# Performance work log

Hardware: AMD Instinct MI355X
Metric: run time of the kernel (lower is better)

Reference implementation:

```python
import jax, jax.numpy as jnp
import numpy as np

PAD_ID = 0


def setup_inputs() -> dict:
    key = jax.random.key(0)
    ks = jax.random.split(key, 14)
    B, S, T = 64, 128, 32
    E = H = 512
    V = 32000
    s = 0.02
    return {
        "trg_tokens": jax.random.randint(ks[0], (B, T), 0, V),
        "src_tokens": jax.random.randint(ks[1], (B, S), 0, V),
        "encoder_out": jax.random.normal(ks[2], (S, B, 2 * H), jnp.float32),
        "hidden": jax.random.normal(ks[3], (B, H), jnp.float32),
        "embed_w": jax.random.normal(ks[4], (V, E), jnp.float32) * s,
        "attn_W": jax.random.normal(ks[5], (H, 2 * H + H), jnp.float32) * s,
        "attn_b": jnp.zeros((H,), jnp.float32),
        "v": jax.random.uniform(ks[6], (H,), jnp.float32),
        "W_ih": jax.random.normal(ks[7], (3 * H, 2 * H + E), jnp.float32) * s,
        "W_hh": jax.random.normal(ks[8], (3 * H, H), jnp.float32) * s,
        "b_ih": jnp.zeros((3 * H,), jnp.float32),
        "b_hh": jnp.zeros((3 * H,), jnp.float32),
        "out_W": jax.random.normal(ks[9], (V, 2 * H + H + E), jnp.float32) * s,
        "out_b": jnp.zeros((V,), jnp.float32),
    }


def reference(trg_tokens, src_tokens, encoder_out, hidden, embed_w, attn_W,
              attn_b, v, W_ih, W_hh, b_ih, b_hh, out_W, out_b):
    # trg_tokens: [B, T], src_tokens: [B, S] (transposed inside, as in torch)
    B, T = trg_tokens.shape
    S = src_tokens.shape[1]
    H = hidden.shape[1]
    V = out_W.shape[0]

    # Embedding with padding_idx -> zero row at PAD_ID
    emb = embed_w.at[PAD_ID].set(0.0)
    mask = (src_tokens != PAD_ID)              # [B, S]
    enc_bt = jnp.transpose(encoder_out, (1, 0, 2))  # [B, S, 2H]
    trg = trg_tokens.T                          # [T, B]

    def step(h, tok):
        x = emb[tok]                            # [B, E]
        # Bahdanau attention
        hrep = jnp.broadcast_to(h[:, None, :], (B, S, H))
        feat = jnp.concatenate([hrep, enc_bt], axis=2)      # [B, S, H+2H]
        energy = jnp.tanh(feat @ attn_W.T + attn_b)          # [B, S, H]
        scores = jnp.einsum('bsd,d->bs', energy, v)          # [B, S]
        scores = jnp.where(mask, scores, -jnp.inf)
        attn = jax.nn.softmax(scores, axis=1)                # [B, S]
        weighted = jnp.einsum('bs,bsd->bd', attn, enc_bt)    # [B, 2H]
        # GRU cell (torch gate order: r, z, n)
        rnn_in = jnp.concatenate([x, weighted], axis=1)      # [B, E+2H]
        gi = rnn_in @ W_ih.T + b_ih                          # [B, 3H]
        gh = h @ W_hh.T + b_hh                               # [B, 3H]
        i_r, i_z, i_n = jnp.split(gi, 3, axis=1)
        h_r, h_z, h_n = jnp.split(gh, 3, axis=1)
        r = jax.nn.sigmoid(i_r + h_r)
        z = jax.nn.sigmoid(i_z + h_z)
        n = jnp.tanh(i_n + r * h_n)
        h_new = (1.0 - z) * n + z * h                        # [B, H]
        # Output projection over cat(output, weighted, x)
        out_feat = jnp.concatenate([h_new, weighted, x], axis=1)  # [B, 2H+H+E]
        logits = out_feat @ out_W.T + out_b                  # [B, V]
        return h_new, logits

    # Teacher forcing ratio = 1.0: inputs are trg[0:T-1]; outputs[0] stays zero
    _, logits_seq = jax.lax.scan(step, hidden, trg[:T - 1])  # [T-1, B, V]
    outputs = jnp.concatenate(
        [jnp.zeros((1, B, V), logits_seq.dtype), logits_seq], axis=0)
    return outputs
```

## Files before the change

### kernel.cpp

```cpp
#include <hip/hip_runtime.h>

typedef __attribute__((ext_vector_type(4))) float f32x4;
typedef __attribute__((ext_vector_type(2))) float f32x2;
typedef __attribute__((ext_vector_type(8))) short s16x8;
typedef __attribute__((ext_vector_type(4))) short s16x4;

#define B_ 64
#define S_ 128
#define T_ 32
#define H_ 512
#define V_ 32000
#define NTILES 2000

#define SY_TILE 32
#define SY_SLOT 64
#define SY_DONE 192

__device__ __forceinline__ unsigned short f2bf(float f) {
  union { float f; unsigned u; } x; x.f = f;
  unsigned r = x.u + 0x7FFFu + ((x.u >> 16) & 1u);
  return (unsigned short)(r >> 16);
}
__device__ __forceinline__ float bf2f(unsigned short u) {
  union { unsigned u; float f; } x; x.u = ((unsigned)u) << 16; return x.f;
}
__device__ __forceinline__ float fast_tanh(float x) {
  float e = __expf(2.0f * x);
  return 1.0f - 2.0f / (e + 1.0f);
}
__device__ __forceinline__ float fast_sig(float x) {
  return 1.0f / (1.0f + __expf(-x));
}
__device__ __forceinline__ void gload16(const void* g, void* l) {
  __builtin_amdgcn_global_load_lds(
      (const __attribute__((address_space(1))) void*)g,
      (__attribute__((address_space(3))) void*)l, 16, 0, 0);
}
__device__ __forceinline__ void gload16nt(const void* g, void* l) {
  __builtin_amdgcn_global_load_lds(
      (const __attribute__((address_space(1))) void*)g,
      (__attribute__((address_space(3))) void*)l, 16, 0, 2);
}

__device__ __forceinline__ unsigned ald(const unsigned* p) {
  return __hip_atomic_load(p, __ATOMIC_RELAXED, __HIP_MEMORY_SCOPE_AGENT);
}
__device__ __forceinline__ void ast(unsigned* p, unsigned v) {
  __hip_atomic_store(p, v, __ATOMIC_RELAXED, __HIP_MEMORY_SCOPE_AGENT);
}
__device__ __forceinline__ void astf(float* p, float v) {
  union { unsigned u; float f; } x; x.f = v; ast((unsigned*)p, x.u);
}

__device__ __forceinline__ void phase_sync(unsigned* sync, int bid,
                                           unsigned st_ph, int nmask,
                                           unsigned wt_ph) {
  __syncthreads();
  if (threadIdx.x == 0)
    __hip_atomic_store(&sync[SY_SLOT + bid], st_ph, __ATOMIC_RELAXED,
                       __HIP_MEMORY_SCOPE_AGENT);
  if (threadIdx.x < 64) {
    const unsigned* p = &sync[SY_SLOT + (threadIdx.x & nmask)];
    while (ald(p) < wt_ph) __builtin_amdgcn_s_sleep(1);
  }
  __syncthreads();
}

template <int OUTBF>
__global__ __launch_bounds__(256) void big_gemm_k(
    const unsigned short* __restrict__ A, int lda,
    const unsigned short* __restrict__ W, const float* __restrict__ bias,
    void* __restrict__ Cv, int Mv, int N, int K) {
  __shared__ unsigned short As[128 * 32];
  __shared__ unsigned short Bs[128 * 32];
  const int t = threadIdx.x;
  const int wave = t >> 6, lane = t & 63;
  const int m0 = blockIdx.x * 128, n0 = blockIdx.y * 128;
  const int wm = (wave & 1) * 64, wn = (wave >> 1) * 64;
  const int fr = lane & 15, fq = lane >> 4;

  f32x4 acc[4][4];
#pragma unroll
  for (int i = 0; i < 4; ++i)
#pragma unroll
    for (int j = 0; j < 4; ++j) acc[i][j] = (f32x4){0.f, 0.f, 0.f, 0.f};

  const int g = (((lane & 3) ^ ((lane >> 3) & 3))) * 8;
  const size_t a_g0 = (size_t)(m0 + wave * 32 + (lane >> 2)) * lda + g;
  const size_t b_g0 = (size_t)(n0 + wave * 32 + (lane >> 2)) * K + g;
  unsigned short* As_w = As + wave * 1024;
  unsigned short* Bs_w = Bs + wave * 1024;
  const int sl = (fq ^ ((fr >> 1) & 3)) * 8;

  for (int kk = 0; kk < K; kk += 32) {
    gload16(A + a_g0 + kk, As_w);
    gload16(A + a_g0 + (size_t)16 * lda + kk, As_w + 512);
    gload16(W + b_g0 + kk, Bs_w);
    gload16(W + b_g0 + (size_t)16 * K + kk, Bs_w + 512);
    __syncthreads();
    s16x8 af[4], bfr[4];
#pragma unroll
    for (int f = 0; f < 4; ++f) {
      af[f] = *(const s16x8*)(As + (wm + f * 16 + fr) * 32 + sl);
      bfr[f] = *(const s16x8*)(Bs + (wn + f * 16 + fr) * 32 + sl);
    }
#pragma unroll
    for (int fm = 0; fm < 4; ++fm)
#pragma unroll
      for (int fn = 0; fn < 4; ++fn)
        acc[fm][fn] = __builtin_amdgcn_mfma_f32_16x16x32_bf16(af[fm], bfr[fn],
                                                              acc[fm][fn], 0, 0, 0);
    __syncthreads();
  }

#pragma unroll
  for (int fn = 0; fn < 4; ++fn) {
    int col = n0 + wn + fn * 16 + fr;
    float bv = bias[col];
#pragma unroll
    for (int fm = 0; fm < 4; ++fm) {
      int rb = m0 + wm + fm * 16 + fq * 4;
#pragma unroll
      for (int i = 0; i < 4; ++i) {
        int r = rb + i;
        if (r < Mv) {
          if (OUTBF)
            ((unsigned short*)Cv)[(size_t)r * N + col] = f2bf(acc[fm][fn][i] + bv);
          else
            ((float*)Cv)[(size_t)r * N + col] = acc[fm][fn][i] + bv;
        }
      }
    }
  }
}

__global__ __launch_bounds__(512) void fused_k(
    float* __restrict__ h, unsigned short* __restrict__ hbf_step,
    float* __restrict__ hgh_step, const unsigned short* __restrict__ Wcomb,
    const unsigned short* __restrict__ encp_bf,
    const unsigned short* __restrict__ enc_bf, const float* __restrict__ v,
    const int* __restrict__ src_tok, const unsigned short* __restrict__ Ww,
    const unsigned short* __restrict__ gix, const float* __restrict__ b_hh,
    unsigned short* __restrict__ Abf, const unsigned short* __restrict__ outW,
    const float* __restrict__ out_b, float* __restrict__ out,
    unsigned* __restrict__ sync) {
  __shared__ __align__(16) char smem[65536];
  const int t = threadIdx.x;
  const int lane = t & 63, w = t >> 6;
  const int fr = lane & 15, fq = lane >> 4;

  if (blockIdx.x < 64) {
    unsigned short* A0 = (unsigned short*)smem;
    unsigned short* A1 = (unsigned short*)(smem + 9216);
    unsigned short* W0 = (unsigned short*)(smem + 18432);
    unsigned short* W1 = (unsigned short*)(smem + 25344);
    unsigned short* Wp1 = (unsigned short*)(smem + 32256);
    float* gsm = (float*)smem;
    float* sc = (float*)(smem + 12288);
    const int j = blockIdx.x;
    const int ar = t >> 3, ak = (t & 7) * 8;
    const int p1_n0 = j * 32;
    const int rowt_p1 = w & 3, colt_p1 = w >> 2;
    const int rowt = (w < 4) ? w : (w - 4);

#pragma unroll
    for (int c = 0; c < 4; ++c) {
      int id = t * 4 + c;
      int r = id >> 6, cc = id & 63;
      s16x8 wv = *(const s16x8*)(Wcomb + (size_t)(p1_n0 + r) * 512 + cc * 8);
      *(s16x8*)(Wp1 + r * 520 + cc * 8) = wv;
    }

    const int wgate = ar >> 4, wdr = ar & 15;
    const int d0 = j * 16;
    const unsigned short* wwrow =
        Ww + (size_t)(wgate * 512 + d0 + wdr) * 1024 + ak;
    s16x8 pwreg[16];
    if (j < 32 && t < 384) {
#pragma unroll
      for (int p = 0; p < 16; ++p) pwreg[p] = *(const s16x8*)(wwrow + p * 64);
    }
    __syncthreads();

    for (int step = 0; step < 31; ++step) {
      const unsigned short* hbfS = hbf_step + (size_t)step * 64 * 512;
      unsigned short* hbfS1 = hbf_step + (size_t)(step + 1) * 64 * 512;
      float* hghS = hgh_step + (size_t)step * 64 * 2048;
      const unsigned ph = 3u * step;

      {
        s16x8 pa[8];
#pragma unroll
        for (int p = 0; p < 8; ++p)
          pa[p] = *(const s16x8*)(hbfS + ar * 512 + p * 64 + ak);
        *(s16x8*)(A0 + ar * 72 + ak) = pa[0];
        __syncthreads();
        f32x4 acc = {0.f, 0.f, 0.f, 0.f};
#pragma unroll
        for (int it = 0; it < 8; ++it) {
          unsigned short* bufR = (it & 1) ? A1 : A0;
          unsigned short* bufW = (it & 1) ? A0 : A1;
          s16x8 a0 = *(const s16x8*)(bufR + (rowt_p1 * 16 + fr) * 72 + fq * 8);
          s16x8 a1 =
              *(const s16x8*)(bufR + (rowt_p1 * 16 + fr) * 72 + 32 + fq * 8);
          if (it < 7) *(s16x8*)(bufW + ar * 72 + ak) = pa[it + 1];
          s16x8 b0 =
              *(const s16x8*)(Wp1 + (colt_p1 * 16 + fr) * 520 + it * 64 + fq * 8);
          s16x8 b1 = *(const s16x8*)(Wp1 + (colt_p1 * 16 + fr) * 520 + it * 64 +
                                     32 + fq * 8);
          acc = __builtin_amdgcn_mfma_f32_16x16x32_bf16(a0, b0, acc, 0, 0, 0);
          acc = __builtin_amdgcn_mfma_f32_16x16x32_bf16(a1, b1, acc, 0, 0, 0);
          __syncthreads();
        }
        int col = p1_n0 + colt_p1 * 16 + fr;
#pragma unroll
        for (int i = 0; i < 4; ++i)
          astf(&hghS[(rowt_p1 * 16 + fq * 4 + i) * 2048 + col], acc[i]);
      }
      phase_sync(sync, j, ph + 1, 15, ph + 1);

      {
        const int b = j;
        const float* hp = hghS + (size_t)b * 2048;
        float vh[8], hh[8];
        {
          f32x4 v0 = *(const f32x4*)(v + lane * 8);
          f32x4 v1 = *(const f32x4*)(v + lane * 8 + 4);
          f32x4 h0 = *(const f32x4*)(hp + lane * 8);
          f32x4 h1 = *(const f32x4*)(hp + lane * 8 + 4);
#pragma unroll
          for (int q = 0; q < 4; ++q) {
            vh[q] = v0[q]; vh[4 + q] = v1[q];
            hh[q] = h0[q]; hh[4 + q] = h1[q];
          }
        }
        for (int s = w * 16; s < w * 16 + 16; ++s) {
          s16x8 e =
              *(const s16x8*)(encp_bf + (size_t)(b * 128 + s) * 512 + lane * 8);
          float p = 0.f;
#pragma unroll
          for (int q = 0; q < 8; ++q)
            p += vh[q] * fast_tanh(hh[q] + bf2f((unsigned short)e[q]));
          for (int m = 32; m; m >>= 1) p += __shfl_xor(p, m);
          if (lane == 0)
            sc[s] = (src_tok[b * 128 + s] != 0) ? p : -__builtin_inff();
        }
        __syncthreads();
        if (t < 64) {
          float a0 = sc[t], a1 = sc[t + 64];
          float mx = fmaxf(a0, a1);
          for (int m = 32; m; m >>= 1) mx = fmaxf(mx, __shfl_xor(mx, m));
          float e0 = __expf(a0 - mx), e1 = __expf(a1 - mx);
          float ssum = e0 + e1;
          for (int m = 32; m; m >>= 1) ssum += __shfl_xor(ssum, m);
          float inv = 1.0f / ssum;
          sc[t] = e0 * inv;
          sc[t + 64] = e1 * inv;
        }
        __syncthreads();
        const int d = t * 2;
        float w0 = 0.f, w1 = 0.f;
#pragma unroll 16
        for (int s = 0; s < 128; ++s) {
          float a = sc[s];
          unsigned u = *(const unsigned*)(enc_bf + (size_t)(b * 128 + s) * 1024 + d);
          union { unsigned u; float f; } lo, hi;
          lo.u = u << 16; hi.u = u & 0xffff0000u;
          w0 += a * lo.f; w1 += a * hi.f;
        }
        unsigned pk = ((unsigned)f2bf(w1) << 16) | (unsigned)f2bf(w0);
        ast((unsigned*)(Abf + (size_t)(step * 64 + b) * 2048 + 512 + d), pk);
      }
      phase_sync(sync, j, ph + 2, 63, ph + 2);

      if (j < 32) {
        const int r0 = step * 64;
        const unsigned short* abrow = Abf + (size_t)(r0 + ar) * 2048 + 512 + ak;
        s16x8 pa[16];
#pragma unroll
        for (int p = 0; p < 16; ++p) pa[p] = *(const s16x8*)(abrow + p * 64);
        *(s16x8*)(A0 + ar * 72 + ak) = pa[0];
        if (t < 384) *(s16x8*)(W0 + ar * 72 + ak) = pwreg[0];
        __syncthreads();
        f32x4 acc0 = {0.f, 0.f, 0.f, 0.f}, acc1 = {0.f, 0.f, 0.f, 0.f};
#pragma unroll
        for (int it = 0; it < 16; ++it) {
          unsigned short* aR = (it & 1) ? A1 : A0;
          unsigned short* wR = (it & 1) ? W1 : W0;
          unsigned short* aW = (it & 1) ? A0 : A1;
          unsigned short* wW = (it & 1) ? W0 : W1;
          s16x8 a0 = *(const s16x8*)(aR + (rowt * 16 + fr) * 72 + fq * 8);
          s16x8 a1 = *(const s16x8*)(aR + (rowt * 16 + fr) * 72 + 32 + fq * 8);
          if (it < 15) {
            *(s16x8*)(aW + ar * 72 + ak) = pa[it + 1];
            if (t < 384) *(s16x8*)(wW + ar * 72 + ak) = pwreg[it + 1];
          }
          if (w < 4) {
            s16x8 b0 = *(const s16x8*)(wR + fr * 72 + fq * 8);
            s16x8 b1 = *(const s16x8*)(wR + fr * 72 + 32 + fq * 8);
            s16x8 c0 = *(const s16x8*)(wR + (32 + fr) * 72 + fq * 8);
            s16x8 c1 = *(const s16x8*)(wR + (32 + fr) * 72 + 32 + fq * 8);
            acc0 = __builtin_amdgcn_mfma_f32_16x16x32_bf16(a0, b0, acc0, 0, 0, 0);
            acc0 = __builtin_amdgcn_mfma_f32_16x16x32_bf16(a1, b1, acc0, 0, 0, 0);
            acc1 = __builtin_amdgcn_mfma_f32_16x16x32_bf16(a0, c0, acc1, 0, 0, 0);
            acc1 = __builtin_amdgcn_mfma_f32_16x16x32_bf16(a1, c1, acc1, 0, 0, 0);
          } else {
            s16x8 b0 = *(const s16x8*)(wR + (16 + fr) * 72 + fq * 8);
            s16x8 b1 = *(const s16x8*)(wR + (16 + fr) * 72 + 32 + fq * 8);
            acc0 = __builtin_amdgcn_mfma_f32_16x16x32_bf16(a0, b0, acc0, 0, 0, 0);
            acc0 = __builtin_amdgcn_mfma_f32_16x16x32_bf16(a1, b1, acc0, 0, 0, 0);
          }
          __syncthreads();
        }
        {
          const int colt0 = (w < 4) ? 0 : 1;
#pragma unroll
          for (int i = 0; i < 4; ++i) {
            int row = rowt * 16 + fq * 4 + i;
            gsm[row * 48 + colt0 * 16 + fr] =
                acc0[i] +
                bf2f(gix[(size_t)(r0 + row) * 1536 + colt0 * 512 + d0 + fr]);
          }
          if (w < 4) {
#pragma unroll
            for (int i = 0; i < 4; ++i) {
              int row = rowt * 16 + fq * 4 + i;
              gsm[row * 48 + 32 + fr] =
                  acc1[i] + bf2f(gix[(size_t)(r0 + row) * 1536 + 1024 + d0 + fr]);
            }
          }
        }
        __syncthreads();
        {
          int e = t * 2;
          int b = e >> 4, dd = e & 15, d = d0 + dd;
          float hv2[2];
          unsigned short hb2[2];
#pragma unroll
          for (int k = 0; k < 2; ++k) {
            float ir = gsm[b * 48 + dd + k];
            float iz = gsm[b * 48 + 16 + dd + k];
            float inn = gsm[b * 48 + 32 + dd + k];
            float hr = hghS[b * 2048 + 512 + d + k] + b_hh[d + k];
            float hz = hghS[b * 2048 + 1024 + d + k] + b_hh[512 + d + k];
            float hn = hghS[b * 2048 + 1536 + d + k] + b_hh[1024 + d + k];
            float r = fast_sig(ir + hr);
            float z = fast_sig(iz + hz);
            float n = fast_tanh(inn + r * hn);
            hv2[k] = (1.0f - z) * n + z * h[b * 512 + d + k];
            hb2[k] = f2bf(hv2[k]);
          }
          h[b * 512 + d] = hv2[0];
          h[b * 512 + d + 1] = hv2[1];
          unsigned pk = ((unsigned)hb2[1] << 16) | (unsigned)hb2[0];
          ast((unsigned*)(hbfS1 + b * 512 + d), pk);
          ast((unsigned*)(Abf + (size_t)(r0 + b) * 2048 + d), pk);
        }
      }
      phase_sync(sync, j, ph + 3, 31, ph + 3);
      if (j == 0 && t == 0) ast(&sync[SY_DONE], (unsigned)(step + 1));
    }
  }

  unsigned short* As2 = (unsigned short*)smem;
  unsigned short* Bs2 = (unsigned short*)(smem + 16384);
  unsigned* shp = (unsigned*)(smem + 65532);
  const int wr = (w >> 2) * 64, wc = (w & 3) * 64;

  int rowA[2], cgA[2], rowB[4], cgB[4];
#pragma unroll
  for (int c = 0; c < 2; ++c) {
    int id = (w * 2 + c) * 64 + lane;
    rowA[c] = id >> 3;
    cgA[c] = ((id & 7) - rowA[c]) & 7;
  }
#pragma unroll
  for (int c = 0; c < 4; ++c) {
    int id = (w * 4 + c) * 64 + lane;
    rowB[c] = id >> 3;
    cgB[c] = ((id & 7) - rowB[c]) & 7;
  }

  for (;;) {
    __syncthreads();
    if (t == 0)
      *shp = __hip_atomic_fetch_add(&sync[SY_TILE], 1u, __ATOMIC_RELAXED,
                                    __HIP_MEMORY_SCOPE_AGENT);
    __syncthreads();
    unsigned idx = *shp;
    if (idx >= NTILES) break;
    int mb = idx / 125;
    int nt = idx - mb * 125;
    int gate = mb * 2 + 1;
    if (gate > 30) gate = 30;
    unsigned need = (unsigned)gate + 1u;
    if (t == 0) {
      while (ald(&sync[SY_DONE]) < need) __builtin_amdgcn_s_sleep(32);
    }
    __syncthreads();

    const int m0 = mb * 128, n0 = nt * 256;
    f32x4 acc[4][4];
#pragma unroll
    for (int i = 0; i < 4; ++i)
#pragma unroll
      for (int jj = 0; jj < 4; ++jj) acc[i][jj] = (f32x4){0.f, 0.f, 0.f, 0.f};

    for (int kk = 0; kk < 2048; kk += 64) {
#pragma unroll
      for (int c = 0; c < 2; ++c)
        gload16(Abf + (size_t)(m0 + rowA[c]) * 2048 + kk + cgA[c] * 8,
                As2 + (w * 2 + c) * 512);
#pragma unroll
      for (int c = 0; c < 4; ++c)
        gload16nt(outW + (size_t)(n0 + rowB[c]) * 2048 + kk + cgB[c] * 8,
                  Bs2 + (w * 4 + c) * 512);
      __syncthreads();
#pragma unroll
      for (int kh = 0; kh < 2; ++kh) {
        int cg = kh * 4 + fq;
        s16x8 af[4], bf_[4];
#pragma unroll
        for (int i = 0; i < 4; ++i) {
          int rr = wr + i * 16 + fr;
          af[i] = *(const s16x8*)(As2 + rr * 64 + (((cg + rr) & 7) * 8));
        }
#pragma unroll
        for (int jj = 0; jj < 4; ++jj) {
          int rr = wc + jj * 16 + fr;
          bf_[jj] = *(const s16x8*)(Bs2 + rr * 64 + (((cg + rr) & 7) * 8));
        }
#pragma unroll
        for (int i = 0; i < 4; ++i)
#pragma unroll
          for (int jj = 0; jj < 4; ++jj)
            acc[i][jj] = __builtin_amdgcn_mfma_f32_16x16x32_bf16(
                af[i], bf_[jj], acc[i][jj], 0, 0, 0);
      }
      __syncthreads();
    }

#pragma unroll
    for (int jj = 0; jj < 4; ++jj) {
      int col = n0 + wc + jj * 16 + fr;
      float bv = out_b[col];
#pragma unroll
      for (int i = 0; i < 4; ++i) {
        int rb = m0 + wr + i * 16 + fq * 4;
#pragma unroll
        for (int ii = 0; ii < 4; ++ii) {
          int r = rb + ii;
          if (r < 1984) out[(size_t)(r + 64) * V_ + col] = acc[i][jj][ii] + bv;
        }
      }
    }
  }
}

__global__ __launch_bounds__(256) void cast_bf16_k(const float* __restrict__ src,
                                                   unsigned short* __restrict__ dst,
                                                   int n4) {
  int i = blockIdx.x * 256 + threadIdx.x;
  if (i >= n4) return;
  f32x4 f = *(const f32x4*)(src + (size_t)i * 4);
  s16x4 o;
#pragma unroll
  for (int q = 0; q < 4; ++q) o[q] = (short)f2bf(f[q]);
  *(s16x4*)(dst + (size_t)i * 4) = o;
}

__global__ __launch_bounds__(256) void enc_cast_k(const float* __restrict__ enc,
                                                  unsigned short* __restrict__ dst) {
  int i = blockIdx.x * 256 + threadIdx.x;
  int n = i * 4;
  int row = n >> 10, d = n & 1023;
  int s = row & (S_ - 1), b = row >> 7;
  f32x4 f = *(const f32x4*)(enc + ((size_t)s * B_ + b) * 1024 + d);
  s16x4 o;
#pragma unroll
  for (int q = 0; q < 4; ++q) o[q] = (short)f2bf(f[q]);
  *(s16x4*)(dst + (size_t)row * 1024 + d) = o;
}

__global__ __launch_bounds__(256) void build_wcomb_k(const float* __restrict__ aW,
                                                     const float* __restrict__ whh,
                                                     unsigned short* __restrict__ dst) {
  int idx = (blockIdx.x * 256 + threadIdx.x) * 4;
  int n = idx >> 9, k = idx & 511;
  const float* src = (n < 512) ? (aW + (size_t)n * 1536 + k)
                               : (whh + (size_t)(n - 512) * 512 + k);
  f32x4 f = *(const f32x4*)src;
  s16x4 o;
#pragma unroll
  for (int q = 0; q < 4; ++q) o[q] = (short)f2bf(f[q]);
  *(s16x4*)(dst + idx) = o;
}

__global__ __launch_bounds__(256) void build_wenc_k(const float* __restrict__ aW,
                                                    unsigned short* __restrict__ dst) {
  int idx = (blockIdx.x * 256 + threadIdx.x) * 4;
  int n = idx >> 10, k = idx & 1023;
  f32x4 f = *(const f32x4*)(aW + (size_t)n * 1536 + 512 + k);
  s16x4 o;
#pragma unroll
  for (int q = 0; q < 4; ++q) o[q] = (short)f2bf(f[q]);
  *(s16x4*)(dst + idx) = o;
}

__global__ __launch_bounds__(256) void build_wxw_k(const float* __restrict__ wih,
                                                   unsigned short* __restrict__ wx,
                                                   unsigned short* __restrict__ ww) {
  int flat = blockIdx.x * 256 + threadIdx.x;
  int n = flat / 384, c4 = (flat % 384) * 4;
  f32x4 f = *(const f32x4*)(wih + (size_t)n * 1536 + c4);
  s16x4 o;
#pragma unroll
  for (int q = 0; q < 4; ++q) o[q] = (short)f2bf(f[q]);
  if (c4 < 512)
    *(s16x4*)(wx + (size_t)n * 512 + c4) = o;
  else
    *(s16x4*)(ww + (size_t)n * 1024 + (c4 - 512)) = o;
}

__global__ __launch_bounds__(256) void hcast_k(const float* __restrict__ hidden,
                                               unsigned short* __restrict__ hbf0) {
  int i = blockIdx.x * 256 + threadIdx.x;
  f32x2 f = *(const f32x2*)(hidden + (size_t)i * 2);
  unsigned pk = ((unsigned)f2bf(f[1]) << 16) | (unsigned)f2bf(f[0]);
  *(unsigned*)(hbf0 + (size_t)i * 2) = pk;
}

__global__ __launch_bounds__(256) void xgather_k(const int* __restrict__ trg,
                                                 const float* __restrict__ embed,
                                                 unsigned short* __restrict__ Abf) {
  int row = blockIdx.x;
  int tt = row >> 6, b = row & 63;
  int tok = trg[b * T_ + tt];
  int d = threadIdx.x * 2;
  unsigned pk = 0;
  if (tok != 0) {
    f32x2 f = *(const f32x2*)(embed + (size_t)tok * H_ + d);
    pk = ((unsigned)f2bf(f[1]) << 16) | (unsigned)f2bf(f[0]);
  }
  *(unsigned*)(Abf + (size_t)row * 2048 + 1536 + d) = pk;
}

extern "C" void kernel_launch(void* const* d_in, const int* in_sizes, int n_in,
                              void* d_out, int out_size, void* d_ws, size_t ws_size,
                              hipStream_t stream) {
  const int* trg = (const int*)d_in[0];
  const int* srt = (const int*)d_in[1];
  const float* enc = (const float*)d_in[2];
  const float* hidden = (const float*)d_in[3];
  const float* embed = (const float*)d_in[4];
  const float* attn_W = (const float*)d_in[5];
  const float* attn_b = (const float*)d_in[6];
  const float* vv = (const float*)d_in[7];
  const float* W_ih = (const float*)d_in[8];
  const float* W_hh = (const float*)d_in[9];
  const float* b_ih = (const float*)d_in[10];
  const float* b_hh = (const float*)d_in[11];
  const float* out_W = (const float*)d_in[12];
  const float* out_b = (const float*)d_in[13];
  float* out = (float*)d_out;

  char* ws = (char*)d_ws;
  size_t off = 0;
  auto alloc = [&](size_t bytes) {
    size_t o = off;
    off += (bytes + 255) & ~(size_t)255;
    return ws + o;
  };

  unsigned short* outW_bf = (unsigned short*)alloc((size_t)V_ * 2048 * 2);
  unsigned short* Abf = (unsigned short*)alloc((size_t)2048 * 2048 * 2);
  unsigned short* enc_bf = (unsigned short*)alloc((size_t)B_ * S_ * 1024 * 2);
  unsigned short* encp_bf = (unsigned short*)alloc((size_t)B_ * S_ * 512 * 2);
  unsigned short* gix_bf = (unsigned short*)alloc((size_t)1984 * 1536 * 2);
  unsigned short* Wcomb = (unsigned short*)alloc((size_t)2048 * 512 * 2);
  unsigned short* Wenc = (unsigned short*)alloc((size_t)512 * 1024 * 2);
  unsigned short* Wx = (unsigned short*)alloc((size_t)1536 * 512 * 2);
  unsigned short* Ww = (unsigned short*)alloc((size_t)1536 * 1024 * 2);
  float* hgh_step = (float*)alloc((size_t)31 * B_ * 2048 * 4);
  unsigned short* hbf_step = (unsigned short*)alloc((size_t)32 * B_ * H_ * 2);
  float* h = (float*)alloc((size_t)B_ * H_ * 4);
  unsigned* syncb = (unsigned*)alloc(8192);

  hipMemsetAsync(out, 0, (size_t)B_ * V_ * 4, stream);
  hipMemsetAsync(syncb, 0, 8192, stream);
  hipMemsetAsync(Abf + (size_t)1984 * 2048, 0, (size_t)64 * 2048 * 2, stream);
  hipMemcpyAsync(h, hidden, (size_t)B_ * H_ * 4, hipMemcpyDeviceToDevice, stream);

  cast_bf16_k<<<(V_ * 2048 / 4 + 255) / 256, 256, 0, stream>>>(out_W, outW_bf,
                                                               V_ * 2048 / 4);
  build_wcomb_k<<<2048 * 512 / 4 / 256, 256, 0, stream>>>(attn_W, W_hh, Wcomb);
  build_wenc_k<<<512 * 1024 / 4 / 256, 256, 0, stream>>>(attn_W, Wenc);
  build_wxw_k<<<1536 * 384 / 256, 256, 0, stream>>>(W_ih, Wx, Ww);
  hcast_k<<<64, 256, 0, stream>>>(hidden, hbf_step);
  enc_cast_k<<<B_ * S_ * 1024 / 4 / 256, 256, 0, stream>>>(enc, enc_bf);
  xgather_k<<<1984, 256, 0, stream>>>(trg, embed, Abf);

  big_gemm_k<1><<<dim3(64, 4), 256, 0, stream>>>(enc_bf, 1024, Wenc, attn_b,
                                                 encp_bf, B_ * S_, 512, 1024);
  big_gemm_k<1><<<dim3(16, 12), 256, 0, stream>>>(Abf + 1536, 2048, Wx, b_ih,
                                                  gix_bf, 1984, 1536, 512);

  fused_k<<<256, 512, 0, stream>>>(h, hbf_step, hgh_step, Wcomb, encp_bf, enc_bf,
                                   vv, srt, Ww, gix_bf, b_hh, Abf, outW_bf, out_b,
                                   out, syncb);
}
```

Baseline: 1.409 ms.

## Split GRU weighted-input GEMM K dimension across 64 blocks with partial-sum handoff

Previously only 32 of the 64 recurrent blocks ran the per-step weighted-context GEMM over K=1024. Now all 64 blocks run it, each covering half of K. The upper-half blocks publish their partial sums to a global buffer, and the lower-half blocks spin-wait on their partner's phase flag before adding the partial and finishing the GRU update. This halves the serial GEMM work per step on the critical path, at the cost of an extra global round-trip and a point-to-point wait.

Result: slower. 1.465 ms (+3.9%).

```diff
diff --git a/kernel.cpp b/kernel.cpp
--- a/kernel.cpp
+++ b/kernel.cpp
@@ -47,6 +47,9 @@
 }
 __device__ __forceinline__ void ast(unsigned* p, unsigned v) {
   __hip_atomic_store(p, v, __ATOMIC_RELAXED, __HIP_MEMORY_SCOPE_AGENT);
+}
+__device__ __forceinline__ float aldf(const float* p) {
+  union { unsigned u; float f; } x; x.u = ald((const unsigned*)p); return x.f;
 }
 __device__ __forceinline__ void astf(float* p, float v) {
   union { unsigned u; float f; } x; x.f = v; ast((unsigned*)p, x.u);
@@ -143,7 +146,7 @@
     const unsigned short* __restrict__ gix, const float* __restrict__ b_hh,
     unsigned short* __restrict__ Abf, const unsigned short* __restrict__ outW,
     const float* __restrict__ out_b, float* __restrict__ out,
-    unsigned* __restrict__ sync) {
+    float* __restrict__ gpart, unsigned* __restrict__ sync) {
   __shared__ __align__(16) char smem[65536];
   const int t = threadIdx.x;
   const int lane = t & 63, w = t >> 6;
@@ -158,6 +161,7 @@
     float* gsm = (float*)smem;
     float* sc = (float*)(smem + 12288);
     const int j = blockIdx.x;
+    const int jj = j & 31, half = j >> 5;
     const int ar = t >> 3, ak = (t & 7) * 8;
     const int p1_n0 = j * 32;
     const int rowt_p1 = w & 3, colt_p1 = w >> 2;
@@ -172,14 +176,15 @@
     }
 
     const int wgate = ar >> 4, wdr = ar & 15;
-    const int d0 = j * 16;
+    const int d0 = jj * 16;
     const unsigned short* wwrow =
-        Ww + (size_t)(wgate * 512 + d0 + wdr) * 1024 + ak;
-    s16x8 pwreg[16];
-    if (j < 32 && t < 384) {
-#pragma unroll
-      for (int p = 0; p < 16; ++p) pwreg[p] = *(const s16x8*)(wwrow + p * 64);
-    }
+        Ww + (size_t)(wgate * 512 + d0 + wdr) * 1024 + ak + half * 512;
+    s16x8 pwreg[8];
+    if (t < 384) {
+#pragma unroll
+      for (int p = 0; p < 8; ++p) pwreg[p] = *(const s16x8*)(wwrow + p * 64);
+    }
+    float* gp = gpart + (size_t)jj * 3072;
     __syncthreads();
 
     for (int step = 0; step < 31; ++step) {
@@ -273,25 +278,26 @@
       }
       phase_sync(sync, j, ph + 2, 63, ph + 2);
 
-      if (j < 32) {
+      {
         const int r0 = step * 64;
-        const unsigned short* abrow = Abf + (size_t)(r0 + ar) * 2048 + 512 + ak;
-        s16x8 pa[16];
-#pragma unroll
-        for (int p = 0; p < 16; ++p) pa[p] = *(const s16x8*)(abrow + p * 64);
+        const unsigned short* abrow =
+            Abf + (size_t)(r0 + ar) * 2048 + 512 + half * 512 + ak;
+        s16x8 pa[8];
+#pragma unroll
+        for (int p = 0; p < 8; ++p) pa[p] = *(const s16x8*)(abrow + p * 64);
         *(s16x8*)(A0 + ar * 72 + ak) = pa[0];
         if (t < 384) *(s16x8*)(W0 + ar * 72 + ak) = pwreg[0];
         __syncthreads();
         f32x4 acc0 = {0.f, 0.f, 0.f, 0.f}, acc1 = {0.f, 0.f, 0.f, 0.f};
 #pragma unroll
-        for (int it = 0; it < 16; ++it) {
+        for (int it = 0; it < 8; ++it) {
           unsigned short* aR = (it & 1) ? A1 : A0;
           unsigned short* wR = (it & 1) ? W1 : W0;
           unsigned short* aW = (it & 1) ? A0 : A1;
           unsigned short* wW = (it & 1) ? W0 : W1;
           s16x8 a0 = *(const s16x8*)(aR + (rowt * 16 + fr) * 72 + fq * 8);
           s16x8 a1 = *(const s16x8*)(aR + (rowt * 16 + fr) * 72 + 32 + fq * 8);
-          if (it < 15) {
+          if (it < 7) {
             *(s16x8*)(aW + ar * 72 + ak) = pa[it + 1];
             if (t < 384) *(s16x8*)(wW + ar * 72 + ak) = pwreg[it + 1];
           }
@@ -312,49 +318,70 @@
           }
           __syncthreads();
         }
-        {
-          const int colt0 = (w < 4) ? 0 : 1;
+        const int colt0 = (w < 4) ? 0 : 1;
+        if (half) {
 #pragma unroll
           for (int i = 0; i < 4; ++i) {
             int row = rowt * 16 + fq * 4 + i;
-            gsm[row * 48 + colt0 * 16 + fr] =
-                acc0[i] +
-                bf2f(gix[(size_t)(r0 + row) * 1536 + colt0 * 512 + d0 + fr]);
+            astf(&gp[row * 48 + colt0 * 16 + fr], acc0[i]);
           }
           if (w < 4) {
 #pragma unroll
             for (int i = 0; i < 4; ++i) {
               int row = rowt * 16 + fq * 4 + i;
+              astf(&gp[row * 48 + 32 + fr], acc1[i]);
+            }
+          }
+        } else {
+          if (t == 0) {
+            while (ald(&sync[SY_SLOT + jj + 32]) < ph + 3)
+              __builtin_amdgcn_s_sleep(1);
+          }
+          __syncthreads();
+#pragma unroll
+          for (int i = 0; i < 4; ++i) {
+            int row = rowt * 16 + fq * 4 + i;
+            float part = aldf(&gp[row * 48 + colt0 * 16 + fr]);
+            gsm[row * 48 + colt0 * 16 + fr] =
+                acc0[i] + part +
+                bf2f(gix[(size_t)(r0 + row) * 1536 + colt0 * 512 + d0 + fr]);
+          }
+          if (w < 4) {
+#pragma unroll
+            for (int i = 0; i < 4; ++i) {
+              int row = rowt * 16 + fq * 4 + i;
+              float part = aldf(&gp[row * 48 + 32 + fr]);
               gsm[row * 48 + 32 + fr] =
-                  acc1[i] + bf2f(gix[(size_t)(r0 + row) * 1536 + 1024 + d0 + fr]);
+                  acc1[i] + part +
+                  bf2f(gix[(size_t)(r0 + row) * 1536 + 1024 + d0 + fr]);
             }
           }
-        }
-        __syncthreads();
-        {
-          int e = t * 2;
-          int b = e >> 4, dd = e & 15, d = d0 + dd;
-          float hv2[2];
-          unsigned short hb2[2];
-#pragma unroll
-          for (int k = 0; k < 2; ++k) {
-            float ir = gsm[b * 48 + dd + k];
-            float iz = gsm[b * 48 + 16 + dd + k];
-            float inn = gsm[b * 48 + 32 + dd + k];
-            float hr = hghS[b * 2048 + 512 + d + k] + b_hh[d + k];
-            float hz = hghS[b * 2048 + 1024 + d + k] + b_hh[512 + d + k];
-            float hn = hghS[b * 2048 + 1536 + d + k] + b_hh[1024 + d + k];
-            float r = fast_sig(ir + hr);
-            float z = fast_sig(iz + hz);
-            float n = fast_tanh(inn + r * hn);
-            hv2[k] = (1.0f - z) * n + z * h[b * 512 + d + k];
-            hb2[k] = f2bf(hv2[k]);
-          }
-          h[b * 512 + d] = hv2[0];
-          h[b * 512 + d + 1] = hv2[1];
-          unsigned pk = ((unsigned)hb2[1] << 16) | (unsigned)hb2[0];
-          ast((unsigned*)(hbfS1 + b * 512 + d), pk);
-          ast((unsigned*)(Abf + (size_t)(r0 + b) * 2048 + d), pk);
+          __syncthreads();
+          {
+            int e = t * 2;
+            int b = e >> 4, dd = e & 15, d = d0 + dd;
+            float hv2[2];
+            unsigned short hb2[2];
+#pragma unroll
+            for (int k = 0; k < 2; ++k) {
+              float ir = gsm[b * 48 + dd + k];
+              float iz = gsm[b * 48 + 16 + dd + k];
+              float inn = gsm[b * 48 + 32 + dd + k];
+              float hr = hghS[b * 2048 + 512 + d + k] + b_hh[d + k];
+              float hz = hghS[b * 2048 + 1024 + d + k] + b_hh[512 + d + k];
+              float hn = hghS[b * 2048 + 1536 + d + k] + b_hh[1024 + d + k];
+              float r = fast_sig(ir + hr);
+              float z = fast_sig(iz + hz);
+              float n = fast_tanh(inn + r * hn);
+              hv2[k] = (1.0f - z) * n + z * h[b * 512 + d + k];
+              hb2[k] = f2bf(hv2[k]);
+            }
+            h[b * 512 + d] = hv2[0];
+            h[b * 512 + d + 1] = hv2[1];
+            unsigned pk = ((unsigned)hb2[1] << 16) | (unsigned)hb2[0];
+            ast((unsigned*)(hbfS1 + b * 512 + d), pk);
+            ast((unsigned*)(Abf + (size_t)(r0 + b) * 2048 + d), pk);
+          }
         }
       }
       phase_sync(sync, j, ph + 3, 31, ph + 3);
@@ -404,7 +431,7 @@
 #pragma unroll
     for (int i = 0; i < 4; ++i)
 #pragma unroll
-      for (int jj = 0; jj < 4; ++jj) acc[i][jj] = (f32x4){0.f, 0.f, 0.f, 0.f};
+      for (int jj2 = 0; jj2 < 4; ++jj2) acc[i][jj2] = (f32x4){0.f, 0.f, 0.f, 0.f};
 
     for (int kk = 0; kk < 2048; kk += 64) {
 #pragma unroll
@@ -426,23 +453,23 @@
           af[i] = *(const s16x8*)(As2 + rr * 64 + (((cg + rr) & 7) * 8));
         }
 #pragma unroll
-        for (int jj = 0; jj < 4; ++jj) {
-          int rr = wc + jj * 16 + fr;
-          bf_[jj] = *(const s16x8*)(Bs2 + rr * 64 + (((cg + rr) & 7) * 8));
+        for (int jj2 = 0; jj2 < 4; ++jj2) {
+          int rr = wc + jj2 * 16 + fr;
+          bf_[jj2] = *(const s16x8*)(Bs2 + rr * 64 + (((cg + rr) & 7) * 8));
         }
 #pragma unroll
         for (int i = 0; i < 4; ++i)
 #pragma unroll
-          for (int jj = 0; jj < 4; ++jj)
-            acc[i][jj] = __builtin_amdgcn_mfma_f32_16x16x32_bf16(
-                af[i], bf_[jj], acc[i][jj], 0, 0, 0);
+          for (int jj2 = 0; jj2 < 4; ++jj2)
+            acc[i][jj2] = __builtin_amdgcn_mfma_f32_16x16x32_bf16(
+                af[i], bf_[jj2], acc[i][jj2], 0, 0, 0);
       }
       __syncthreads();
     }
 
 #pragma unroll
-    for (int jj = 0; jj < 4; ++jj) {
-      int col = n0 + wc + jj * 16 + fr;
+    for (int jj2 = 0; jj2 < 4; ++jj2) {
+      int col = n0 + wc + jj2 * 16 + fr;
       float bv = out_b[col];
 #pragma unroll
       for (int i = 0; i < 4; ++i) {
@@ -450,7 +477,7 @@
 #pragma unroll
         for (int ii = 0; ii < 4; ++ii) {
           int r = rb + ii;
-          if (r < 1984) out[(size_t)(r + 64) * V_ + col] = acc[i][jj][ii] + bv;
+          if (r < 1984) out[(size_t)(r + 64) * V_ + col] = acc[i][jj2][ii] + bv;
         }
       }
     }
@@ -584,6 +611,7 @@
   float* hgh_step = (float*)alloc((size_t)31 * B_ * 2048 * 4);
   unsigned short* hbf_step = (unsigned short*)alloc((size_t)32 * B_ * H_ * 2);
   float* h = (float*)alloc((size_t)B_ * H_ * 4);
+  float* gpart = (float*)alloc((size_t)32 * 3072 * 4);
   unsigned* syncb = (unsigned*)alloc(8192);
 
   hipMemsetAsync(out, 0, (size_t)B_ * V_ * 4, stream);
@@ -607,5 +635,5 @@
 
   fused_k<<<256, 512, 0, stream>>>(h, hbf_step, hgh_step, Wcomb, encp_bf, enc_bf,
                                    vv, srt, Ww, gix_bf, b_hh, Abf, outW_bf, out_b,
-                                   out, syncb);
-}
+                                   out, gpart, syncb);
+}
```
